# Kernel optimization log

Measured on AMD Instinct MI355X. Metric: run time of the kernel, lower is better.

## Reference

```python
import jax, jax.numpy as jnp
import numpy as np

N_NODES = 100000
N_EDGES = 1600000
IN_DIM = 64
OUT_DIM = 64


def setup_inputs() -> dict:
    key = jax.random.key(0)
    k1, k2, k3, k4 = jax.random.split(key, 4)
    x = jax.random.normal(k1, (N_NODES, IN_DIM), dtype=jnp.float32)
    edge_index = jax.random.randint(k2, (2, N_EDGES), 0, N_NODES, dtype=jnp.int64)
    # nn.Linear-style init: U(-1/sqrt(in), 1/sqrt(in))
    lim = 1.0 / np.sqrt(IN_DIM)
    W = jax.random.uniform(k3, (OUT_DIM, IN_DIM), dtype=jnp.float32, minval=-lim, maxval=lim)
    b = jax.random.uniform(k4, (OUT_DIM,), dtype=jnp.float32, minval=-lim, maxval=lim)
    return {"x": x, "edge_index": edge_index, "W": W, "b": b}


def reference(x, edge_index, W, b):
    n = x.shape[0]
    row, col = edge_index[0], edge_index[1]
    # gather source features along edges, scatter-add into destination rows
    agg = jax.ops.segment_sum(x[col], row, num_segments=n)  # [n, in_dim]
    deg = jax.ops.segment_sum(jnp.ones(row.shape[0], dtype=x.dtype), row, num_segments=n)
    deg = jnp.clip(deg, 1.0, None)[:, None]  # [n, 1]
    out = agg / deg
    return out @ W.T + b  # [n, out_dim]
```

## Files before the change

kernel.cpp:

```cpp
#include <hip/hip_runtime.h>
#include <hip/hip_bf16.h>
#include <hip/hip_fp16.h>

#define DIM 64
#define NPART 8

__global__ void detect_kernel(const unsigned int* __restrict__ ei, int* __restrict__ flag) {
    const int lane = threadIdx.x & 63;
    const unsigned int hi = ei[2 * lane + 1];
    const unsigned long long ball = __ballot(hi != 0u);
    if (threadIdx.x == 0) *flag = (ball == 0ULL) ? 1 : 0;
}

__global__ void __launch_bounds__(256) cvt_idx_kernel(
    const void* __restrict__ eiv, int* __restrict__ rows32, int* __restrict__ cols32,
    int nE, const int* __restrict__ flag) {
    const int e = blockIdx.x * 256 + threadIdx.x;
    if (e >= nE) return;
    if (*flag) {
        const long long* ei = (const long long*)eiv;
        rows32[e] = (int)ei[e];
        cols32[e] = (int)ei[nE + e];
    } else {
        const int* ei = (const int*)eiv;
        rows32[e] = ei[e];
        cols32[e] = ei[nE + e];
    }
}

__global__ void __launch_bounds__(256) convert_kernel(
    const float4* __restrict__ x, ushort4* __restrict__ xh, int n4) {
    const int i = blockIdx.x * 256 + threadIdx.x;
    if (i >= n4) return;
    const float4 v = x[i];
    ushort4 o;
    o.x = __half_as_ushort(__float2half(v.x));
    o.y = __half_as_ushort(__float2half(v.y));
    o.z = __half_as_ushort(__float2half(v.z));
    o.w = __half_as_ushort(__float2half(v.w));
    xh[i] = o;
}

__global__ void __launch_bounds__(256) hist32_kernel(
    const int* __restrict__ rows32, int* __restrict__ cnt, int nE) {
    const int base = (blockIdx.x * 256 + threadIdx.x) * 4;
    if (base + 3 < nE) {
        const int4 r = *(const int4*)&rows32[base];
        atomicAdd(&cnt[r.x], 1);
        atomicAdd(&cnt[r.y], 1);
        atomicAdd(&cnt[r.z], 1);
        atomicAdd(&cnt[r.w], 1);
    } else {
        for (int k = 0; k < 4; ++k)
            if (base + k < nE) atomicAdd(&cnt[rows32[base + k]], 1);
    }
}

__global__ void __launch_bounds__(256) scan1_kernel(
    const int* __restrict__ cnt, int* __restrict__ cursor,
    int* __restrict__ blksums, int n) {
    __shared__ int tmp[256];
    const int t = threadIdx.x;
    const int base = blockIdx.x * 1024 + t * 4;
    int v0 = (base + 0 < n) ? cnt[base + 0] : 0;
    int v1 = (base + 1 < n) ? cnt[base + 1] : 0;
    int v2 = (base + 2 < n) ? cnt[base + 2] : 0;
    int v3 = (base + 3 < n) ? cnt[base + 3] : 0;
    const int s = v0 + v1 + v2 + v3;
    tmp[t] = s;
    __syncthreads();
    for (int off = 1; off < 256; off <<= 1) {
        int v = 0;
        if (t >= off) v = tmp[t - off];
        __syncthreads();
        tmp[t] += v;
        __syncthreads();
    }
    const int excl = tmp[t] - s;
    if (t == 255) blksums[blockIdx.x] = tmp[255];
    if (base + 0 < n) cursor[base + 0] = excl;
    if (base + 1 < n) cursor[base + 1] = excl + v0;
    if (base + 2 < n) cursor[base + 2] = excl + v0 + v1;
    if (base + 3 < n) cursor[base + 3] = excl + v0 + v1 + v2;
}

__global__ void __launch_bounds__(1024) scan2_kernel(int* __restrict__ blksums, int nblk) {
    __shared__ int tmp[1024];
    const int t = threadIdx.x;
    const int v = (t < nblk) ? blksums[t] : 0;
    tmp[t] = v;
    __syncthreads();
    for (int off = 1; off < 1024; off <<= 1) {
        int u = 0;
        if (t >= off) u = tmp[t - off];
        __syncthreads();
        tmp[t] += u;
        __syncthreads();
    }
    if (t < nblk) blksums[t] = tmp[t] - v;
}

__global__ void __launch_bounds__(256) scan3_kernel(
    int* __restrict__ cursor, const int* __restrict__ blksums, int n) {
    const int add = blksums[blockIdx.x];
    const int base = blockIdx.x * 1024 + threadIdx.x * 4;
    if (base + 0 < n) cursor[base + 0] += add;
    if (base + 1 < n) cursor[base + 1] += add;
    if (base + 2 < n) cursor[base + 2] += add;
    if (base + 3 < n) cursor[base + 3] += add;
}

__global__ void __launch_bounds__(256) build_part32_kernel(
    const int* __restrict__ rows32, const int* __restrict__ cols32,
    int* __restrict__ cursor, int* __restrict__ scol, int nE, int n) {
    const int p  = blockIdx.x & (NPART - 1);
    const int q  = blockIdx.x / NPART;
    const int nq = gridDim.x / NPART;
    const unsigned bound = (unsigned)((n + NPART - 1) / NPART);
    const unsigned lo    = (unsigned)p * bound;
    const int stride = nq * 256;
    for (int e = q * 256 + (int)threadIdx.x; e < nE; e += stride) {
        const int r = rows32[e];
        if ((unsigned)r - lo < bound) {
            const int pos = atomicAdd(&cursor[r], 1);
            scol[pos] = cols32[e];
        }
    }
}

__global__ void __launch_bounds__(256) gather_finalize_kernel(
    const __half* __restrict__ xh, const int* __restrict__ scol,
    const int* __restrict__ cursor, const int* __restrict__ cnt,
    const float* __restrict__ W, const float* __restrict__ b,
    float* __restrict__ out, int n) {
    __shared__ __align__(16) float rowbuf[4][DIM];
    const int group = threadIdx.x >> 6;
    const int lane  = threadIdx.x & 63;
    const int wid   = (int)((blockIdx.x * blockDim.x + threadIdx.x) >> 6);
    const int nw    = (int)((gridDim.x * blockDim.x) >> 6);

    float wc[DIM];
    #pragma unroll
    for (int k4 = 0; k4 < DIM / 4; ++k4) {
        float4 w4 = *(const float4*)&W[(size_t)lane * DIM + k4 * 4];
        wc[k4 * 4 + 0] = w4.x; wc[k4 * 4 + 1] = w4.y;
        wc[k4 * 4 + 2] = w4.z; wc[k4 * 4 + 3] = w4.w;
    }
    const float bl = b[lane];

    for (int r = wid; r < n; r += nw) {
        const int k   = cnt[r];
        const int end = cursor[r];
        const int s   = end - k;
        float a0 = 0.0f, a1 = 0.0f;
        int j = 0;
        for (; j + 3 < k; j += 4) {
            const int c0 = scol[s + j + 0];
            const int c1 = scol[s + j + 1];
            const int c2 = scol[s + j + 2];
            const int c3 = scol[s + j + 3];
            const float v0 = __half2float(xh[(size_t)c0 * DIM + lane]);
            const float v1 = __half2float(xh[(size_t)c1 * DIM + lane]);
            const float v2 = __half2float(xh[(size_t)c2 * DIM + lane]);
            const float v3 = __half2float(xh[(size_t)c3 * DIM + lane]);
            a0 += v0; a1 += v1; a0 += v2; a1 += v3;
        }
        for (; j < k; ++j) {
            const int c = scol[s + j];
            a0 += __half2float(xh[(size_t)c * DIM + lane]);
        }
        const float dg   = (k > 0) ? (float)k : 1.0f;
        const float mean = (a0 + a1) / dg;

        rowbuf[group][lane] = mean;
        float dot = bl;
        #pragma unroll
        for (int k4 = 0; k4 < DIM / 4; ++k4) {
            const float4 m4 = *(const float4*)&rowbuf[group][k4 * 4];
            dot += m4.x * wc[k4 * 4 + 0];
            dot += m4.y * wc[k4 * 4 + 1];
            dot += m4.z * wc[k4 * 4 + 2];
            dot += m4.w * wc[k4 * 4 + 3];
        }
        out[(size_t)r * DIM + lane] = dot;
    }
}

__global__ void __launch_bounds__(256) hist_kernel(
    const void* __restrict__ eiv, int* __restrict__ cnt,
    int nE, const int* __restrict__ flag) {
    const int base = (blockIdx.x * 256 + threadIdx.x) * 4;
    if (base >= nE) return;
    if (*flag) {
        const long long* ei = (const long long*)eiv;
        #pragma unroll
        for (int k = 0; k < 4; ++k)
            if (base + k < nE) atomicAdd(&cnt[(int)ei[base + k]], 1);
    } else {
        const int* ei = (const int*)eiv;
        #pragma unroll
        for (int k = 0; k < 4; ++k)
            if (base + k < nE) atomicAdd(&cnt[ei[base + k]], 1);
    }
}

__global__ void __launch_bounds__(256) build_part_ei_kernel(
    const void* __restrict__ eiv, int* __restrict__ cursor,
    int* __restrict__ scol, int nE, int n, const int* __restrict__ flag) {
    const int p  = blockIdx.x & (NPART - 1);
    const int q  = blockIdx.x / NPART;
    const int nq = gridDim.x / NPART;
    const unsigned bound = (unsigned)((n + NPART - 1) / NPART);
    const unsigned lo    = (unsigned)p * bound;
    const int stride = nq * 256;
    const int is64 = *flag;
    if (is64) {
        const long long* ei = (const long long*)eiv;
        for (int e = q * 256 + (int)threadIdx.x; e < nE; e += stride) {
            const int r = (int)ei[e];
            if ((unsigned)r - lo < bound) {
                const int pos = atomicAdd(&cursor[r], 1);
                scol[pos] = (int)ei[nE + e];
            }
        }
    } else {
        const int* ei = (const int*)eiv;
        for (int e = q * 256 + (int)threadIdx.x; e < nE; e += stride) {
            const int r = ei[e];
            if ((unsigned)r - lo < bound) {
                const int pos = atomicAdd(&cursor[r], 1);
                scol[pos] = ei[nE + e];
            }
        }
    }
}

__global__ void __launch_bounds__(256) gather_finalize_f32_kernel(
    const float* __restrict__ x, const int* __restrict__ scol,
    const int* __restrict__ cursor, const int* __restrict__ cnt,
    const float* __restrict__ W, const float* __restrict__ b,
    float* __restrict__ out, int n) {
    __shared__ __align__(16) float rowbuf[4][DIM];
    const int group = threadIdx.x >> 6;
    const int lane  = threadIdx.x & 63;
    const int wid   = (int)((blockIdx.x * blockDim.x + threadIdx.x) >> 6);
    const int nw    = (int)((gridDim.x * blockDim.x) >> 6);
    float wc[DIM];
    #pragma unroll
    for (int k4 = 0; k4 < DIM / 4; ++k4) {
        float4 w4 = *(const float4*)&W[(size_t)lane * DIM + k4 * 4];
        wc[k4 * 4 + 0] = w4.x; wc[k4 * 4 + 1] = w4.y;
        wc[k4 * 4 + 2] = w4.z; wc[k4 * 4 + 3] = w4.w;
    }
    const float bl = b[lane];
    for (int r = wid; r < n; r += nw) {
        const int k   = cnt[r];
        const int end = cursor[r];
        const int s   = end - k;
        float a0 = 0.0f, a1 = 0.0f;
        int j = 0;
        for (; j + 3 < k; j += 4) {
            a0 += x[(size_t)scol[s + j + 0] * DIM + lane];
            a1 += x[(size_t)scol[s + j + 1] * DIM + lane];
            a0 += x[(size_t)scol[s + j + 2] * DIM + lane];
            a1 += x[(size_t)scol[s + j + 3] * DIM + lane];
        }
        for (; j < k; ++j) a0 += x[(size_t)scol[s + j] * DIM + lane];
        const float dg   = (k > 0) ? (float)k : 1.0f;
        const float mean = (a0 + a1) / dg;
        rowbuf[group][lane] = mean;
        float dot = bl;
        #pragma unroll
        for (int k4 = 0; k4 < DIM / 4; ++k4) {
            const float4 m4 = *(const float4*)&rowbuf[group][k4 * 4];
            dot += m4.x * wc[k4 * 4 + 0];
            dot += m4.y * wc[k4 * 4 + 1];
            dot += m4.z * wc[k4 * 4 + 2];
            dot += m4.w * wc[k4 * 4 + 3];
        }
        out[(size_t)r * DIM + lane] = dot;
    }
}

extern "C" void kernel_launch(void* const* d_in, const int* in_sizes, int n_in,
                              void* d_out, int out_size, void* d_ws, size_t ws_size,
                              hipStream_t stream) {
    const float* x  = (const float*)d_in[0];
    const void*  ei = (const void*)d_in[1];
    const float* W  = (const float*)d_in[2];
    const float* b  = (const float*)d_in[3];
    float* out = (float*)d_out;

    const int n  = in_sizes[0] / DIM;
    const int nE = in_sizes[1] / 2;

    int* wsI     = (int*)d_ws;
    int* cnt     = wsI;
    int* cursor  = wsI + n;
    int* blksums = wsI + 2 * n;
    int* flag    = wsI + 2 * n + 1024;
    int* scol    = wsI + 2 * n + 1088;
    __half* xh   = (__half*)(wsI + 2 * n + 1088 + nE);
    int* rows32  = wsI + 2 * n + 1088 + nE + n * (DIM / 2);
    int* cols32  = rows32 + nE;

    const size_t need_csr  = ((size_t)2 * n + 1088 + (size_t)nE) * sizeof(int);
    const size_t need_fp16 = need_csr + (size_t)n * DIM * sizeof(__half);
    const size_t need_full = need_fp16 + (size_t)2 * nE * sizeof(int);

    if (ws_size < need_csr) return;

    const int nblk = (n + 1023) / 1024;
    const bool fp16 = (ws_size >= need_fp16);
    const bool full = (ws_size >= need_full);

    detect_kernel<<<1, 64, 0, stream>>>((const unsigned int*)ei, flag);
    hipMemsetAsync(cnt, 0, (size_t)n * sizeof(int), stream);
    if (fp16) {
        const int n4 = n * DIM / 4;
        convert_kernel<<<(n4 + 255) / 256, 256, 0, stream>>>(
            (const float4*)x, (ushort4*)xh, n4);
    }

    if (full) {
        cvt_idx_kernel<<<(nE + 255) / 256, 256, 0, stream>>>(ei, rows32, cols32, nE, flag);
        hist32_kernel<<<(nE / 4 + 255) / 256, 256, 0, stream>>>(rows32, cnt, nE);
    } else {
        hist_kernel<<<(nE / 4 + 255) / 256, 256, 0, stream>>>(ei, cnt, nE, flag);
    }

    scan1_kernel<<<nblk, 256, 0, stream>>>(cnt, cursor, blksums, n);
    scan2_kernel<<<1, 1024, 0, stream>>>(blksums, nblk);
    scan3_kernel<<<nblk, 256, 0, stream>>>(cursor, blksums, n);

    if (full) {
        build_part32_kernel<<<2048, 256, 0, stream>>>(rows32, cols32, cursor, scol, nE, n);
    } else {
        build_part_ei_kernel<<<2048, 256, 0, stream>>>(ei, cursor, scol, nE, n, flag);
    }

    if (fp16) {
        gather_finalize_kernel<<<2048, 256, 0, stream>>>(xh, scol, cursor, cnt, W, b, out, n);
    } else {
        gather_finalize_f32_kernel<<<2048, 256, 0, stream>>>(x, scol, cursor, cnt, W, b, out, n);
    }
}
```

Measured before the change: 352.9 us.

## Fuse index conversion with histogram, vectorize gather by quarter-wave, fp16 dot2 projection

Merges the index-narrowing and degree-histogram passes into one kernel that reads edge_index with vector loads, removing one full pass over the edges. The gather kernel now has each quarter-wave fetch a different neighbor's row as 8-byte vectors, processing four neighbors per load step, and reduces the partial sums with cross-lane shuffles. The mean vector and W are stored in fp16, and the projection uses packed dot2 instructions with W pre-converted by a small kernel. Rounding the mean and the weights to fp16 lowers accuracy, and W stays in 32 registers per lane.

```diff
diff --git a/kernel.cpp b/kernel.cpp
--- a/kernel.cpp
+++ b/kernel.cpp
@@ -4,28 +4,31 @@
 
 #define DIM 64
 #define NPART 8
+
+typedef _Float16 half2_t __attribute__((ext_vector_type(2)));
+
+#if defined(__has_builtin)
+#if __has_builtin(__builtin_amdgcn_fdot2)
+#define HAVE_FDOT2 1
+#endif
+#endif
+
+__device__ __forceinline__ float dot2acc(unsigned int mu, unsigned int wu, float acc) {
+#ifdef HAVE_FDOT2
+    return __builtin_amdgcn_fdot2(__builtin_bit_cast(half2_t, mu),
+                                  __builtin_bit_cast(half2_t, wu), acc, false);
+#else
+    const float2 mf = __half22float2(*(const __half2*)&mu);
+    const float2 wf = __half22float2(*(const __half2*)&wu);
+    return acc + mf.x * wf.x + mf.y * wf.y;
+#endif
+}
 
 __global__ void detect_kernel(const unsigned int* __restrict__ ei, int* __restrict__ flag) {
     const int lane = threadIdx.x & 63;
     const unsigned int hi = ei[2 * lane + 1];
     const unsigned long long ball = __ballot(hi != 0u);
     if (threadIdx.x == 0) *flag = (ball == 0ULL) ? 1 : 0;
-}
-
-__global__ void __launch_bounds__(256) cvt_idx_kernel(
-    const void* __restrict__ eiv, int* __restrict__ rows32, int* __restrict__ cols32,
-    int nE, const int* __restrict__ flag) {
-    const int e = blockIdx.x * 256 + threadIdx.x;
-    if (e >= nE) return;
-    if (*flag) {
-        const long long* ei = (const long long*)eiv;
-        rows32[e] = (int)ei[e];
-        cols32[e] = (int)ei[nE + e];
-    } else {
-        const int* ei = (const int*)eiv;
-        rows32[e] = ei[e];
-        cols32[e] = ei[nE + e];
-    }
 }
 
 __global__ void __launch_bounds__(256) convert_kernel(
@@ -41,18 +44,55 @@
     xh[i] = o;
 }
 
-__global__ void __launch_bounds__(256) hist32_kernel(
-    const int* __restrict__ rows32, int* __restrict__ cnt, int nE) {
+__global__ void __launch_bounds__(256) cvtW_kernel(
+    const float* __restrict__ W, unsigned int* __restrict__ wh2, int n2) {
+    const int i = blockIdx.x * 256 + threadIdx.x;
+    if (i >= n2) return;
+    const float2 f = ((const float2*)W)[i];
+    const __half2 h = __floats2half2_rn(f.x, f.y);
+    wh2[i] = *(const unsigned int*)&h;
+}
+
+__global__ void __launch_bounds__(256) prep_kernel(
+    const void* __restrict__ eiv, int* __restrict__ rows32, int* __restrict__ cols32,
+    int* __restrict__ cnt, int nE, const int* __restrict__ flag) {
     const int base = (blockIdx.x * 256 + threadIdx.x) * 4;
+    if (base >= nE) return;
     if (base + 3 < nE) {
-        const int4 r = *(const int4*)&rows32[base];
-        atomicAdd(&cnt[r.x], 1);
-        atomicAdd(&cnt[r.y], 1);
-        atomicAdd(&cnt[r.z], 1);
-        atomicAdd(&cnt[r.w], 1);
+        int4 rr, cc;
+        if (*flag) {
+            const long long* ei = (const long long*)eiv;
+            const longlong2 r01 = *(const longlong2*)&ei[base];
+            const longlong2 r23 = *(const longlong2*)&ei[base + 2];
+            const longlong2 c01 = *(const longlong2*)&ei[nE + base];
+            const longlong2 c23 = *(const longlong2*)&ei[nE + base + 2];
+            rr = make_int4((int)r01.x, (int)r01.y, (int)r23.x, (int)r23.y);
+            cc = make_int4((int)c01.x, (int)c01.y, (int)c23.x, (int)c23.y);
+        } else {
+            const int* ei = (const int*)eiv;
+            rr = *(const int4*)&ei[base];
+            cc = *(const int4*)&ei[nE + base];
+        }
+        *(int4*)&rows32[base] = rr;
+        *(int4*)&cols32[base] = cc;
+        atomicAdd(&cnt[rr.x], 1);
+        atomicAdd(&cnt[rr.y], 1);
+        atomicAdd(&cnt[rr.z], 1);
+        atomicAdd(&cnt[rr.w], 1);
     } else {
-        for (int k = 0; k < 4; ++k)
-            if (base + k < nE) atomicAdd(&cnt[rows32[base + k]], 1);
+        for (int k = 0; k < 4 && base + k < nE; ++k) {
+            int r, c;
+            if (*flag) {
+                const long long* ei = (const long long*)eiv;
+                r = (int)ei[base + k]; c = (int)ei[nE + base + k];
+            } else {
+                const int* ei = (const int*)eiv;
+                r = ei[base + k]; c = ei[nE + base + k];
+            }
+            rows32[base + k] = r;
+            cols32[base + k] = c;
+            atomicAdd(&cnt[r], 1);
+        }
     }
 }
 
@@ -128,59 +168,84 @@
     }
 }
 
-__global__ void __launch_bounds__(256) gather_finalize_kernel(
+__global__ void __launch_bounds__(256) gather_finalize_q_kernel(
     const __half* __restrict__ xh, const int* __restrict__ scol,
     const int* __restrict__ cursor, const int* __restrict__ cnt,
-    const float* __restrict__ W, const float* __restrict__ b,
+    const unsigned int* __restrict__ wh2, const float* __restrict__ b,
     float* __restrict__ out, int n) {
-    __shared__ __align__(16) float rowbuf[4][DIM];
-    const int group = threadIdx.x >> 6;
-    const int lane  = threadIdx.x & 63;
-    const int wid   = (int)((blockIdx.x * blockDim.x + threadIdx.x) >> 6);
-    const int nw    = (int)((gridDim.x * blockDim.x) >> 6);
-
-    float wc[DIM];
+    __shared__ __align__(16) unsigned int rowh[4][32];
+    const int tid   = threadIdx.x;
+    const int group = tid >> 6;
+    const int lane  = tid & 63;
+    const int q     = lane >> 4;
+    const int s16   = lane & 15;
+    const int wid   = (int)((blockIdx.x * 256 + tid) >> 6);
+    const int nw    = (int)((gridDim.x * 256) >> 6);
+
+    unsigned int wcu[32];
     #pragma unroll
-    for (int k4 = 0; k4 < DIM / 4; ++k4) {
-        float4 w4 = *(const float4*)&W[(size_t)lane * DIM + k4 * 4];
-        wc[k4 * 4 + 0] = w4.x; wc[k4 * 4 + 1] = w4.y;
-        wc[k4 * 4 + 2] = w4.z; wc[k4 * 4 + 3] = w4.w;
-    }
+    for (int i = 0; i < 32; ++i) wcu[i] = wh2[lane * 32 + i];
+    #pragma unroll
+    for (int i = 0; i < 32; ++i) asm volatile("" : "+v"(wcu[i]));
+
     const float bl = b[lane];
 
-    for (int r = wid; r < n; r += nw) {
+    for (int r0 = wid; r0 < n; r0 += nw) {
+        const int r   = __builtin_amdgcn_readfirstlane(r0);
         const int k   = cnt[r];
         const int end = cursor[r];
         const int s   = end - k;
-        float a0 = 0.0f, a1 = 0.0f;
+        float a0 = 0.f, a1 = 0.f, a2 = 0.f, a3 = 0.f;
         int j = 0;
-        for (; j + 3 < k; j += 4) {
-            const int c0 = scol[s + j + 0];
-            const int c1 = scol[s + j + 1];
-            const int c2 = scol[s + j + 2];
-            const int c3 = scol[s + j + 3];
-            const float v0 = __half2float(xh[(size_t)c0 * DIM + lane]);
-            const float v1 = __half2float(xh[(size_t)c1 * DIM + lane]);
-            const float v2 = __half2float(xh[(size_t)c2 * DIM + lane]);
-            const float v3 = __half2float(xh[(size_t)c3 * DIM + lane]);
-            a0 += v0; a1 += v1; a0 += v2; a1 += v3;
+        for (; j + 7 < k; j += 8) {
+            const int cA = scol[s + j + q];
+            const int cB = scol[s + j + 4 + q];
+            const uint2 uA = *(const uint2*)(xh + ((size_t)cA << 6) + (s16 << 2));
+            const uint2 uB = *(const uint2*)(xh + ((size_t)cB << 6) + (s16 << 2));
+            float2 f;
+            f = __half22float2(*(const __half2*)&uA.x); a0 += f.x; a1 += f.y;
+            f = __half22float2(*(const __half2*)&uA.y); a2 += f.x; a3 += f.y;
+            f = __half22float2(*(const __half2*)&uB.x); a0 += f.x; a1 += f.y;
+            f = __half22float2(*(const __half2*)&uB.y); a2 += f.x; a3 += f.y;
+        }
+        if (j + 3 < k) {
+            const int cA = scol[s + j + q];
+            const uint2 uA = *(const uint2*)(xh + ((size_t)cA << 6) + (s16 << 2));
+            float2 f;
+            f = __half22float2(*(const __half2*)&uA.x); a0 += f.x; a1 += f.y;
+            f = __half22float2(*(const __half2*)&uA.y); a2 += f.x; a3 += f.y;
+            j += 4;
         }
         for (; j < k; ++j) {
             const int c = scol[s + j];
-            a0 += __half2float(xh[(size_t)c * DIM + lane]);
-        }
-        const float dg   = (k > 0) ? (float)k : 1.0f;
-        const float mean = (a0 + a1) / dg;
-
-        rowbuf[group][lane] = mean;
+            if (q == 0) {
+                const uint2 u = *(const uint2*)(xh + ((size_t)c << 6) + (s16 << 2));
+                float2 f;
+                f = __half22float2(*(const __half2*)&u.x); a0 += f.x; a1 += f.y;
+                f = __half22float2(*(const __half2*)&u.y); a2 += f.x; a3 += f.y;
+            }
+        }
+        a0 += __shfl_xor(a0, 16); a0 += __shfl_xor(a0, 32);
+        a1 += __shfl_xor(a1, 16); a1 += __shfl_xor(a1, 32);
+        a2 += __shfl_xor(a2, 16); a2 += __shfl_xor(a2, 32);
+        a3 += __shfl_xor(a3, 16); a3 += __shfl_xor(a3, 32);
+        const float inv = 1.0f / ((k > 0) ? (float)k : 1.0f);
+        if (q == 0) {
+            const __half2 m01 = __floats2half2_rn(a0 * inv, a1 * inv);
+            const __half2 m23 = __floats2half2_rn(a2 * inv, a3 * inv);
+            uint2 mu;
+            mu.x = *(const unsigned int*)&m01;
+            mu.y = *(const unsigned int*)&m23;
+            *(uint2*)&rowh[group][s16 * 2] = mu;
+        }
         float dot = bl;
         #pragma unroll
-        for (int k4 = 0; k4 < DIM / 4; ++k4) {
-            const float4 m4 = *(const float4*)&rowbuf[group][k4 * 4];
-            dot += m4.x * wc[k4 * 4 + 0];
-            dot += m4.y * wc[k4 * 4 + 1];
-            dot += m4.z * wc[k4 * 4 + 2];
-            dot += m4.w * wc[k4 * 4 + 3];
+        for (int i4 = 0; i4 < 8; ++i4) {
+            const uint4 mm = *(const uint4*)&rowh[group][i4 * 4];
+            dot = dot2acc(mm.x, wcu[i4 * 4 + 0], dot);
+            dot = dot2acc(mm.y, wcu[i4 * 4 + 1], dot);
+            dot = dot2acc(mm.z, wcu[i4 * 4 + 2], dot);
+            dot = dot2acc(mm.w, wcu[i4 * 4 + 3], dot);
         }
         out[(size_t)r * DIM + lane] = dot;
     }
@@ -213,8 +278,7 @@
     const unsigned bound = (unsigned)((n + NPART - 1) / NPART);
     const unsigned lo    = (unsigned)p * bound;
     const int stride = nq * 256;
-    const int is64 = *flag;
-    if (is64) {
+    if (*flag) {
         const long long* ei = (const long long*)eiv;
         for (int e = q * 256 + (int)threadIdx.x; e < nE; e += stride) {
             const int r = (int)ei[e];
@@ -300,31 +364,30 @@
     int* blksums = wsI + 2 * n;
     int* flag    = wsI + 2 * n + 1024;
     int* scol    = wsI + 2 * n + 1088;
-    __half* xh   = (__half*)(wsI + 2 * n + 1088 + nE);
-    int* rows32  = wsI + 2 * n + 1088 + nE + n * (DIM / 2);
+    __half* xh   = (__half*)(scol + nE);
+    int* rows32  = scol + nE + n * (DIM / 2);
     int* cols32  = rows32 + nE;
+    unsigned int* wh2 = (unsigned int*)(cols32 + nE);
 
     const size_t need_csr  = ((size_t)2 * n + 1088 + (size_t)nE) * sizeof(int);
-    const size_t need_fp16 = need_csr + (size_t)n * DIM * sizeof(__half);
-    const size_t need_full = need_fp16 + (size_t)2 * nE * sizeof(int);
+    const size_t need_full = need_csr + (size_t)n * DIM * sizeof(__half)
+                           + (size_t)2 * nE * sizeof(int)
+                           + (size_t)(DIM * DIM / 2) * sizeof(int);
 
     if (ws_size < need_csr) return;
 
     const int nblk = (n + 1023) / 1024;
-    const bool fp16 = (ws_size >= need_fp16);
     const bool full = (ws_size >= need_full);
 
     detect_kernel<<<1, 64, 0, stream>>>((const unsigned int*)ei, flag);
     hipMemsetAsync(cnt, 0, (size_t)n * sizeof(int), stream);
-    if (fp16) {
+
+    if (full) {
         const int n4 = n * DIM / 4;
         convert_kernel<<<(n4 + 255) / 256, 256, 0, stream>>>(
             (const float4*)x, (ushort4*)xh, n4);
-    }
-
-    if (full) {
-        cvt_idx_kernel<<<(nE + 255) / 256, 256, 0, stream>>>(ei, rows32, cols32, nE, flag);
-        hist32_kernel<<<(nE / 4 + 255) / 256, 256, 0, stream>>>(rows32, cnt, nE);
+        cvtW_kernel<<<(DIM * DIM / 2 + 255) / 256, 256, 0, stream>>>(W, wh2, DIM * DIM / 2);
+        prep_kernel<<<(nE / 4 + 255) / 256, 256, 0, stream>>>(ei, rows32, cols32, cnt, nE, flag);
     } else {
         hist_kernel<<<(nE / 4 + 255) / 256, 256, 0, stream>>>(ei, cnt, nE, flag);
     }
@@ -335,13 +398,9 @@
 
     if (full) {
         build_part32_kernel<<<2048, 256, 0, stream>>>(rows32, cols32, cursor, scol, nE, n);
+        gather_finalize_q_kernel<<<2048, 256, 0, stream>>>(xh, scol, cursor, cnt, wh2, b, out, n);
     } else {
         build_part_ei_kernel<<<2048, 256, 0, stream>>>(ei, cursor, scol, nE, n, flag);
-    }
-
-    if (fp16) {
-        gather_finalize_kernel<<<2048, 256, 0, stream>>>(xh, scol, cursor, cnt, W, b, out, n);
-    } else {
         gather_finalize_f32_kernel<<<2048, 256, 0, stream>>>(x, scol, cursor, cnt, W, b, out, n);
     }
 }
```

Measured after the change: 307.1 us. 1.15x faster.
